# Optimization experiments

Hardware: AMD Instinct MI355X
Metric: run time of the kernel (lower is better)

Reference implementation:

```python
import jax, jax.numpy as jnp
import numpy as np

S, B, H = 2048, 16, 512      # seq_len, batch, hidden_size
L = 4096                     # total labels across batch
SMAX = 16                    # max span length
LAB = 256                    # label_size
V = 32000                    # len(voc)


def setup_inputs() -> dict:
    key = jax.random.key(0)
    ks = jax.random.split(key, 10)
    hidden = jax.random.normal(ks[0], (S, B, H), jnp.float32)
    begins = jax.random.randint(ks[1], (L,), 1, S - SMAX - 1)          # >=1 so begin-1 valid
    lens = jax.random.randint(ks[2], (L,), 1, SMAX + 1)                # span length in [1, SMAX]
    ends = begins + lens                                               # < S so hidden[end] valid
    bids = jax.random.randint(ks[3], (L,), 0, B)
    tags = jax.random.randint(ks[4], (L,), 0, V)
    sc = 0.02
    W1 = jax.random.normal(ks[5], (3 * H, LAB), jnp.float32) * sc
    b1 = jnp.zeros((LAB,), jnp.float32)
    W2 = jax.random.normal(ks[6], (LAB, LAB), jnp.float32) * sc
    b2 = jnp.zeros((LAB,), jnp.float32)
    Wo = jax.random.normal(ks[7], (LAB, V), jnp.float32) * sc
    bo = jnp.zeros((V,), jnp.float32)
    return dict(hidden=hidden, begins=begins, ends=ends, bids=bids, tags=tags,
                W1=W1, b1=b1, W2=W2, b2=b2, Wo=Wo, bo=bo)


def reference(hidden, begins, ends, bids, tags, W1, b1, W2, b2, Wo, bo):
    # --- batched span embed: gather + masked mean + boundary concat ---
    pos = begins[:, None] + jnp.arange(SMAX)            # [L, SMAX]
    valid = (pos < ends[:, None]).astype(hidden.dtype)  # [L, SMAX]
    posc = jnp.minimum(pos, S - 1)
    g = hidden[posc, bids[:, None]]                     # [L, SMAX, H] gather
    span_len = (ends - begins).astype(hidden.dtype)[:, None]
    mean = (g * valid[..., None]).sum(axis=1) / span_len           # [L, H]
    left = hidden[begins - 1, bids]                                 # [L, H]
    right = hidden[ends, bids]                                      # [L, H]
    span_emb = jnp.concatenate([left, mean, right], axis=-1)        # [L, 3H]
    # --- hidden2feature: Linear -> sigmoid -> Linear (dropout = eval identity) ---
    feat = jax.nn.sigmoid(span_emb @ W1 + b1) @ W2 + b2             # [L, LAB]
    # --- SoftmaxLoss: -log_softmax(h2o(feat)).gather(tags).mean() per label ---
    logp = jax.nn.log_softmax(feat @ Wo + bo, axis=-1)              # [L, V]
    per_label = -logp[jnp.arange(L), tags]                          # one tag per label
    return per_label.sum() / (L + 1e-5)
```

## Files before the change

kernel.cpp:

```cpp
#include <hip/hip_runtime.h>
#include <math.h>

#define S 2048
#define B 16
#define H 512
#define L 4096
#define SMAX 16
#define LAB 256
#define V 32000
#define NCH 250
#define LOG2E 1.44269504f

typedef __attribute__((ext_vector_type(8))) short short8;
typedef __attribute__((ext_vector_type(4))) float float4v;

__device__ inline ushort f2bf(float x) {
  union { float f; unsigned u; } c; c.f = x;
  unsigned r = c.u + 0x7fffu + ((c.u >> 16) & 1u);
  return (ushort)(r >> 16);
}
__device__ inline float bf2f(ushort h) {
  union { unsigned u; float f; } c; c.u = ((unsigned)h) << 16;
  return c.f;
}

__global__ __launch_bounds__(256) void prep_kernel(
    const float* __restrict__ hidden, const int* __restrict__ begins,
    const int* __restrict__ ends, const int* __restrict__ bids,
    ushort* __restrict__ spanb, const float* __restrict__ W1,
    ushort* __restrict__ W1b, const float* __restrict__ W2,
    ushort* __restrict__ W2b, const float* __restrict__ Wo,
    ushort* __restrict__ Wob) {
  __shared__ ushort tile[64 * 72];
  int bid = blockIdx.x;
  int t = threadIdx.x;

  if (bid < 2048) {
    int sub = t >> 7, tt = t & 127;
    int l = bid * 2 + sub;
    int b = bids[l], s0 = begins[l], s1 = ends[l];
    const float4* hidv = (const float4*)hidden;
    float4 lf = hidv[((size_t)(s0 - 1) * B + b) * 128 + tt];
    float4 rf = hidv[((size_t)s1 * B + b) * 128 + tt];
    float4 m = make_float4(0.f, 0.f, 0.f, 0.f);
    int len = s1 - s0;
    #pragma unroll
    for (int j = 0; j < SMAX; ++j) {
      float4 g = hidv[((size_t)(s0 + j) * B + b) * 128 + tt];
      if (j < len) { m.x += g.x; m.y += g.y; m.z += g.z; m.w += g.w; }
    }
    float inv = 1.0f / (float)len;
    ushort* sp = spanb + (size_t)l * 1536;
    ushort4 u;
    u.x = f2bf(lf.x); u.y = f2bf(lf.y); u.z = f2bf(lf.z); u.w = f2bf(lf.w);
    *(ushort4*)&sp[tt * 4] = u;
    u.x = f2bf(m.x * inv); u.y = f2bf(m.y * inv);
    u.z = f2bf(m.z * inv); u.w = f2bf(m.w * inv);
    *(ushort4*)&sp[512 + tt * 4] = u;
    u.x = f2bf(rf.x); u.y = f2bf(rf.y); u.z = f2bf(rf.z); u.w = f2bf(rf.w);
    *(ushort4*)&sp[1024 + tt * 4] = u;
    return;
  }

  const float* src; ushort* dst; int K, N, n0, k0; bool wo = false;
  if (bid < 2144) {
    int u = bid - 2048; src = W1; dst = W1b; K = 1536; N = 256;
    n0 = (u & 3) * 64; k0 = (u >> 2) * 64;
  } else if (bid < 2160) {
    int u = bid - 2144; src = W2; dst = W2b; K = 256; N = 256;
    n0 = (u & 3) * 64; k0 = (u >> 2) * 64;
  } else {
    int u = bid - 2160; src = Wo; dst = Wob; K = 256; N = V;
    n0 = (u % 500) * 64; k0 = (u / 500) * 64; wo = true;
  }
  #pragma unroll
  for (int p = 0; p < 16; ++p) {
    int k = p * 4 + (t >> 6);
    int n = t & 63;
    tile[n * 72 + k] = f2bf(src[(size_t)(k0 + k) * N + n0 + n]);
  }
  __syncthreads();
  if (!wo) {
    #pragma unroll
    for (int p = 0; p < 2; ++p) {
      int idx = p * 256 + t;
      int n = idx >> 3, c = idx & 7;
      *(uint4*)&dst[(size_t)(n0 + n) * K + k0 + c * 8] =
          *(const uint4*)&tile[n * 72 + c * 8];
    }
  } else {
    #pragma unroll
    for (int p = 0; p < 2; ++p) {
      int idx = p * 256 + t;
      int n = idx >> 3, c8 = idx & 7;
      int v = n0 + n, k = k0 + c8 * 8;
      int c = v >> 7, nt = (v >> 4) & 7, lr = v & 15;
      int kh = k >> 7, k4 = (k >> 5) & 3, lq = (k >> 3) & 3;
      size_t f = ((((size_t)c * 2 + kh) * 4 + k4) * 8 + nt) * 64 + lq * 16 + lr;
      *(uint4*)&dst[f * 8] = *(const uint4*)&tile[n * 72 + c8 * 8];
    }
  }
}

__global__ __launch_bounds__(256) void feat_mfma_kernel(
    const ushort* __restrict__ spanb, const ushort* __restrict__ W1b,
    const float* __restrict__ b1, const ushort* __restrict__ W2b,
    const float* __restrict__ b2, ushort* __restrict__ featb,
    float* __restrict__ zsum, float* __restrict__ out) {
  __shared__ ushort Hs[16 * 264];
  int tid = threadIdx.x;
  if (blockIdx.x == 0 && tid == 0) *out = 0.f;
  if (tid < 16) zsum[blockIdx.x * 16 + tid] = 0.f;
  int w = tid >> 6, lane = tid & 63;
  int lr = lane & 15, lq = lane >> 4;
  int l0 = blockIdx.x * 16;

  const short8* arow = (const short8*)(spanb + (size_t)(l0 + lr) * 1536 + lq * 8);
  const short8* brow[4];
  #pragma unroll
  for (int nt = 0; nt < 4; ++nt)
    brow[nt] = (const short8*)(W1b + (size_t)(w * 64 + nt * 16 + lr) * 1536 + lq * 8);

  float4v acc[4];
  float4v zero = {0.f, 0.f, 0.f, 0.f};
  #pragma unroll
  for (int nt = 0; nt < 4; ++nt) acc[nt] = zero;

  short8 af[2], bf[2][4];
  af[0] = arow[0];
  #pragma unroll
  for (int nt = 0; nt < 4; ++nt) bf[0][nt] = brow[nt][0];

  #pragma unroll
  for (int s = 0; s < 48; ++s) {
    int cur = s & 1, nxt = cur ^ 1;
    if (s < 47) {
      af[nxt] = arow[(s + 1) * 4];
      #pragma unroll
      for (int nt = 0; nt < 4; ++nt) bf[nxt][nt] = brow[nt][(s + 1) * 4];
    }
    #pragma unroll
    for (int nt = 0; nt < 4; ++nt)
      acc[nt] = __builtin_amdgcn_mfma_f32_16x16x32_bf16(
          af[cur], bf[cur][nt], acc[nt], 0, 0, 0);
  }

  {
    #pragma unroll
    for (int nt = 0; nt < 4; ++nt) {
      float b1v = b1[w * 64 + nt * 16 + lr];
      #pragma unroll
      for (int r = 0; r < 4; ++r) {
        int row = lq * 4 + r;
        float h = 1.0f / (1.0f + __expf(-(acc[nt][r] + b1v)));
        Hs[row * 264 + w * 64 + nt * 16 + lr] = f2bf(h);
      }
    }
  }
  __syncthreads();

  const short8* wrow[4];
  #pragma unroll
  for (int nt = 0; nt < 4; ++nt)
    wrow[nt] = (const short8*)(W2b + (size_t)(w * 64 + nt * 16 + lr) * 256 + lq * 8);

  float4v acc2[4];
  #pragma unroll
  for (int nt = 0; nt < 4; ++nt) acc2[nt] = zero;

  short8 bf2[2][4];
  #pragma unroll
  for (int nt = 0; nt < 4; ++nt) bf2[0][nt] = wrow[nt][0];

  #pragma unroll
  for (int s = 0; s < 8; ++s) {
    int cur = s & 1, nxt = cur ^ 1;
    if (s < 7) {
      #pragma unroll
      for (int nt = 0; nt < 4; ++nt) bf2[nxt][nt] = wrow[nt][(s + 1) * 4];
    }
    short8 af2 = *(const short8*)&Hs[lr * 264 + s * 32 + lq * 8];
    #pragma unroll
    for (int nt = 0; nt < 4; ++nt)
      acc2[nt] = __builtin_amdgcn_mfma_f32_16x16x32_bf16(
          af2, bf2[cur][nt], acc2[nt], 0, 0, 0);
  }

  {
    #pragma unroll
    for (int nt = 0; nt < 4; ++nt) {
      float b2v = b2[w * 64 + nt * 16 + lr];
      #pragma unroll
      for (int r = 0; r < 4; ++r) {
        int row = lq * 4 + r;
        int col = w * 64 + nt * 16 + lr;
        featb[(size_t)(l0 + row) * 256 + col] = f2bf(acc2[nt][r] + b2v);
      }
    }
  }
}

__global__ __launch_bounds__(512, 4) void logits2_kernel(
    const ushort* __restrict__ featb, const ushort* __restrict__ Wob,
    const float* __restrict__ bo, float* __restrict__ zsum) {
  __shared__ ushort Blds[2][16384];
  int tid = threadIdx.x;
  int w = tid >> 6, lane = tid & 63;
  int lr = lane & 15, lq = lane >> 4;
  int l0 = blockIdx.x * 256;
  int v0 = blockIdx.y * 128;

  const short8* aptr[2];
  #pragma unroll
  for (int mt = 0; mt < 2; ++mt)
    aptr[mt] = (const short8*)(featb +
        (size_t)(l0 + w * 32 + mt * 16 + lr) * 256 + lq * 8);

  float4v acc[2][8];
  float4v zero = {0.f, 0.f, 0.f, 0.f};
  #pragma unroll
  for (int mt = 0; mt < 2; ++mt)
    #pragma unroll
    for (int nt = 0; nt < 8; ++nt) acc[mt][nt] = zero;

  short8 af[2][2];
  #pragma unroll
  for (int mt = 0; mt < 2; ++mt) af[0][mt] = aptr[mt][0];

#define STAGE_HALF(buf, kh)                                                   \
  {                                                                           \
    const uint4* src4 = (const uint4*)(Wob +                                  \
        (size_t)blockIdx.y * 32768 + (size_t)(kh) * 16384);                   \
    _Pragma("unroll")                                                         \
    for (int p = 0; p < 4; ++p) {                                             \
      int idx = p * 512 + tid;                                                \
      __builtin_amdgcn_global_load_lds(                                       \
          (const __attribute__((address_space(1))) unsigned int*)(src4 + idx),\
          (__attribute__((address_space(3))) unsigned int*)                   \
              &Blds[buf][(size_t)idx * 8],                                    \
          16, 0, 0);                                                          \
    }                                                                         \
  }

#define KG_BLOCK(buf, kh)                                                     \
  _Pragma("unroll")                                                           \
  for (int k4 = 0; k4 < 4; ++k4) {                                            \
    int kg = (kh) * 4 + k4;                                                   \
    int cur = kg & 1, nxt = cur ^ 1;                                          \
    if (kg < 7) {                                                             \
      _Pragma("unroll")                                                       \
      for (int mt = 0; mt < 2; ++mt)                                          \
        af[nxt][mt] = aptr[mt][(kg + 1) * 4];                                 \
    }                                                                         \
    short8 bf[8];                                                             \
    _Pragma("unroll")                                                         \
    for (int nt = 0; nt < 8; ++nt)                                            \
      bf[nt] = *(const short8*)                                               \
          &Blds[buf][(size_t)(((k4 * 8 + nt) * 64) + lane) * 8];              \
    __builtin_amdgcn_s_setprio(1);                                            \
    _Pragma("unroll")                                                         \
    for (int mt = 0; mt < 2; ++mt)                                            \
      _Pragma("unroll")                                                       \
      for (int nt = 0; nt < 8; ++nt)                                          \
        acc[mt][nt] = __builtin_amdgcn_mfma_f32_16x16x32_bf16(                \
            af[cur][mt], bf[nt], acc[mt][nt], 0, 0, 0);                       \
    __builtin_amdgcn_s_setprio(0);                                            \
  }

  STAGE_HALF(0, 0);
  __syncthreads();
  STAGE_HALF(1, 1);
  KG_BLOCK(0, 0);
  __syncthreads();
  KG_BLOCK(1, 1);

#undef STAGE_HALF
#undef KG_BLOCK

  float bov[8];
  #pragma unroll
  for (int nt = 0; nt < 8; ++nt)
    bov[nt] = bo[v0 + nt * 16 + lr] * LOG2E;
  float z[2][4];
  #pragma unroll
  for (int mt = 0; mt < 2; ++mt)
    #pragma unroll
    for (int r = 0; r < 4; ++r) z[mt][r] = 0.f;
  #pragma unroll
  for (int mt = 0; mt < 2; ++mt)
    #pragma unroll
    for (int nt = 0; nt < 8; ++nt)
      #pragma unroll
      for (int r = 0; r < 4; ++r)
        z[mt][r] += exp2f(fmaf(acc[mt][nt][r], LOG2E, bov[nt]));
  #pragma unroll
  for (int mt = 0; mt < 2; ++mt)
    #pragma unroll
    for (int r = 0; r < 4; ++r) {
      #pragma unroll
      for (int off = 1; off < 16; off <<= 1)
        z[mt][r] += __shfl_xor(z[mt][r], off);
    }
  if (lr == 0) {
    #pragma unroll
    for (int mt = 0; mt < 2; ++mt)
      #pragma unroll
      for (int r = 0; r < 4; ++r)
        atomicAdd(&zsum[l0 + w * 32 + mt * 16 + lq * 4 + r], z[mt][r]);
  }
}

__global__ __launch_bounds__(256) void final_kernel(
    const ushort* __restrict__ featb, const ushort* __restrict__ Wob,
    const float* __restrict__ bo, const int* __restrict__ tags,
    const float* __restrict__ zsum, float* __restrict__ out) {
  int tid = threadIdx.x;
  int w = tid >> 6, lane = tid & 63;
  int lb = blockIdx.x * 64;
  float psum = 0.f;
  for (int i = 0; i < 16; ++i) {
    int l = lb + w * 16 + i;
    int tg = tags[l];
    int c = tg >> 7, nt = (tg >> 4) & 7, lr = tg & 15;
    int k0 = lane << 2;
    int kh = k0 >> 7, k4 = (k0 >> 5) & 3, lq = (k0 >> 3) & 3, e = k0 & 7;
    size_t f = ((((size_t)c * 2 + kh) * 4 + k4) * 8 + nt) * 64 + lq * 16 + lr;
    ushort4 wa = *(const ushort4*)&Wob[f * 8 + e];
    ushort4 fa = *(const ushort4*)&featb[(size_t)l * 256 + k0];
    float s = bf2f(fa.x) * bf2f(wa.x) + bf2f(fa.y) * bf2f(wa.y) +
              bf2f(fa.z) * bf2f(wa.z) + bf2f(fa.w) * bf2f(wa.w);
    #pragma unroll
    for (int off = 1; off < 64; off <<= 1) s += __shfl_xor(s, off);
    if (lane == 0)
      psum += logf(zsum[l]) - (s + bo[tg]);
  }
  __shared__ float wsum[4];
  if (lane == 0) wsum[w] = psum;
  __syncthreads();
  if (tid == 0) {
    float v = (wsum[0] + wsum[1] + wsum[2] + wsum[3]) *
              (1.0f / (4096.0f + 1e-5f));
    atomicAdd(out, v);
  }
}

extern "C" void kernel_launch(void* const* d_in, const int* in_sizes, int n_in,
                              void* d_out, int out_size, void* d_ws,
                              size_t ws_size, hipStream_t stream) {
  const float* hidden = (const float*)d_in[0];
  const int* begins = (const int*)d_in[1];
  const int* ends = (const int*)d_in[2];
  const int* bids = (const int*)d_in[3];
  const int* tags = (const int*)d_in[4];
  const float* W1 = (const float*)d_in[5];
  const float* b1 = (const float*)d_in[6];
  const float* W2 = (const float*)d_in[7];
  const float* b2 = (const float*)d_in[8];
  const float* Wo = (const float*)d_in[9];
  const float* bo = (const float*)d_in[10];
  float* out = (float*)d_out;

  ushort* featb = (ushort*)d_ws;
  ushort* Wob = featb + (size_t)L * 256;
  ushort* spanb = Wob + (size_t)V * 256;
  ushort* W1b = spanb + (size_t)L * 1536;
  ushort* W2b = W1b + (size_t)256 * 1536;
  float* zsum = (float*)(W2b + (size_t)256 * 256);

  prep_kernel<<<4160, 256, 0, stream>>>(hidden, begins, ends, bids, spanb,
                                        W1, W1b, W2, W2b, Wo, Wob);
  feat_mfma_kernel<<<256, 256, 0, stream>>>(spanb, W1b, b1, W2b, b2, featb,
                                            zsum, out);
  logits2_kernel<<<dim3(16, NCH), 512, 0, stream>>>(featb, Wob, bo, zsum);
  final_kernel<<<L / 64, 256, 0, stream>>>(featb, Wob, bo, tags, zsum, out);
}
```

Baseline: 286.9 us.

## Replace zsum atomics with per-chunk partial sums and coalesce Wo repack stores

```diff
diff --git a/kernel.cpp b/kernel.cpp
--- a/kernel.cpp
+++ b/kernel.cpp
@@ -92,12 +92,16 @@
     #pragma unroll
     for (int p = 0; p < 2; ++p) {
       int idx = p * 256 + t;
-      int n = idx >> 3, c8 = idx & 7;
-      int v = n0 + n, k = k0 + c8 * 8;
-      int c = v >> 7, nt = (v >> 4) & 7, lr = v & 15;
-      int kh = k >> 7, k4 = (k >> 5) & 3, lq = (k >> 3) & 3;
+      int fr = idx >> 6, slot = idx & 63;
+      int ntl = fr & 3, k4l = fr >> 2;
+      int lq = slot >> 4, lr = slot & 15;
+      int v = n0 + ntl * 16 + lr;
+      int k = k0 + k4l * 32 + lq * 8;
+      int c = v >> 7, nt = (v >> 4) & 7;
+      int kh = k >> 7, k4 = (k >> 5) & 3;
       size_t f = ((((size_t)c * 2 + kh) * 4 + k4) * 8 + nt) * 64 + lq * 16 + lr;
-      *(uint4*)&dst[f * 8] = *(const uint4*)&tile[n * 72 + c8 * 8];
+      *(uint4*)&dst[f * 8] =
+          *(const uint4*)&tile[(ntl * 16 + lr) * 72 + k4l * 32 + lq * 8];
     }
   }
 }
@@ -106,11 +110,10 @@
     const ushort* __restrict__ spanb, const ushort* __restrict__ W1b,
     const float* __restrict__ b1, const ushort* __restrict__ W2b,
     const float* __restrict__ b2, ushort* __restrict__ featb,
-    float* __restrict__ zsum, float* __restrict__ out) {
+    float* __restrict__ out) {
   __shared__ ushort Hs[16 * 264];
   int tid = threadIdx.x;
   if (blockIdx.x == 0 && tid == 0) *out = 0.f;
-  if (tid < 16) zsum[blockIdx.x * 16 + tid] = 0.f;
   int w = tid >> 6, lane = tid & 63;
   int lr = lane & 15, lq = lane >> 4;
   int l0 = blockIdx.x * 16;
@@ -202,7 +205,7 @@
 
 __global__ __launch_bounds__(512, 4) void logits2_kernel(
     const ushort* __restrict__ featb, const ushort* __restrict__ Wob,
-    const float* __restrict__ bo, float* __restrict__ zsum) {
+    const float* __restrict__ bo, float* __restrict__ pz) {
   __shared__ ushort Blds[2][16384];
   int tid = threadIdx.x;
   int w = tid >> 6, lane = tid & 63;
@@ -302,21 +305,38 @@
         z[mt][r] += __shfl_xor(z[mt][r], off);
     }
   if (lr == 0) {
-    #pragma unroll
-    for (int mt = 0; mt < 2; ++mt)
-      #pragma unroll
-      for (int r = 0; r < 4; ++r)
-        atomicAdd(&zsum[l0 + w * 32 + mt * 16 + lq * 4 + r], z[mt][r]);
+    int ch = blockIdx.y;
+    #pragma unroll
+    for (int mt = 0; mt < 2; ++mt) {
+      float4 v4;
+      v4.x = z[mt][0]; v4.y = z[mt][1]; v4.z = z[mt][2]; v4.w = z[mt][3];
+      *(float4*)&pz[(size_t)ch * L + l0 + w * 32 + mt * 16 + lq * 4] = v4;
+    }
   }
 }
 
 __global__ __launch_bounds__(256) void final_kernel(
     const ushort* __restrict__ featb, const ushort* __restrict__ Wob,
     const float* __restrict__ bo, const int* __restrict__ tags,
-    const float* __restrict__ zsum, float* __restrict__ out) {
+    const float* __restrict__ pz, float* __restrict__ out) {
+  __shared__ float zp[4][64];
+  __shared__ float zl[64];
+  __shared__ float wsum[4];
   int tid = threadIdx.x;
   int w = tid >> 6, lane = tid & 63;
   int lb = blockIdx.x * 64;
+
+  {
+    float zs = 0.f;
+    for (int c = w; c < NCH; c += 4)
+      zs += pz[(size_t)c * L + lb + lane];
+    zp[w][lane] = zs;
+  }
+  __syncthreads();
+  if (w == 0)
+    zl[lane] = zp[0][lane] + zp[1][lane] + zp[2][lane] + zp[3][lane];
+  __syncthreads();
+
   float psum = 0.f;
   for (int i = 0; i < 16; ++i) {
     int l = lb + w * 16 + i;
@@ -332,9 +352,8 @@
     #pragma unroll
     for (int off = 1; off < 64; off <<= 1) s += __shfl_xor(s, off);
     if (lane == 0)
-      psum += logf(zsum[l]) - (s + bo[tg]);
-  }
-  __shared__ float wsum[4];
+      psum += logf(zl[w * 16 + i]) - (s + bo[tg]);
+  }
   if (lane == 0) wsum[w] = psum;
   __syncthreads();
   if (tid == 0) {
@@ -365,12 +384,12 @@
   ushort* spanb = Wob + (size_t)V * 256;
   ushort* W1b = spanb + (size_t)L * 1536;
   ushort* W2b = W1b + (size_t)256 * 1536;
-  float* zsum = (float*)(W2b + (size_t)256 * 256);
+  float* pz = (float*)spanb;
 
   prep_kernel<<<4160, 256, 0, stream>>>(hidden, begins, ends, bids, spanb,
                                         W1, W1b, W2, W2b, Wo, Wob);
   feat_mfma_kernel<<<256, 256, 0, stream>>>(spanb, W1b, b1, W2b, b2, featb,
-                                            zsum, out);
-  logits2_kernel<<<dim3(16, NCH), 512, 0, stream>>>(featb, Wob, bo, zsum);
-  final_kernel<<<L / 64, 256, 0, stream>>>(featb, Wob, bo, tags, zsum, out);
-}
+                                            out);
+  logits2_kernel<<<dim3(16, NCH), 512, 0, stream>>>(featb, Wob, bo, pz);
+  final_kernel<<<L / 64, 256, 0, stream>>>(featb, Wob, bo, tags, pz, out);
+}
```

After: 291.7 us. Within noise of the previous version (+1.7%).
